# Kernel tuning notes

Hardware: AMD Instinct MI355X
Metric: run time of the kernel (lower is better)

Reference implementation:

```python
import jax, jax.numpy as jnp
import numpy as np

TOP_K = 2
NOISE_STDDEV = 1.0


def setup_inputs() -> dict:
    key = jax.random.key(0)
    k1, k2, k3, k4 = jax.random.split(key, 4)
    N, D, E = 16384, 2048, 64
    x = jax.random.normal(k1, (N, D), dtype=jnp.float32)
    W_gate = jax.random.normal(k2, (E, D), dtype=jnp.float32) * (1.0 / np.sqrt(D))
    W_noise = jax.random.normal(k3, (E, D), dtype=jnp.float32) * (1.0 / np.sqrt(D))
    noise = jax.random.normal(k4, (N, E), dtype=jnp.float32)
    return {"x": x, "W_gate": W_gate, "W_noise": W_noise, "noise": noise}


def reference(x, W_gate, W_noise, noise):
    # clean gating logits: [N, E]
    clean_logits = jnp.einsum("nd,ed->ne", x, W_gate)
    # noise scale via softplus of second projection (training mode)
    noise_scale = jax.nn.softplus(jnp.einsum("nd,ed->ne", x, W_noise))
    noisy_logits = clean_logits + noise_scale * noise * NOISE_STDDEV
    # top-k selection then softmax over the k selected logits
    top_k_logits, top_k_indices = jax.lax.top_k(noisy_logits, TOP_K)
    combined_weights = jax.nn.softmax(top_k_logits, axis=-1)
    return (combined_weights, top_k_indices, clean_logits)
```

## Files before the change

### kernel.cpp

```cpp
#include <hip/hip_runtime.h>
#include <math.h>


constexpr int NROWS = 16384;
constexpr int DDIM  = 2048;
constexpr int EDIM  = 64;
constexpr int BM    = 64;
constexpr int NKS   = 64;
constexpr int LSTR  = 132;
constexpr int IDX_OFF   = NROWS * 2;
constexpr int CLEAN_OFF = NROWS * 4;
constexpr size_t WPACK = 262144;
constexpr int BUFSZ = 24576;
constexpr int NBUF  = 4;

typedef _Float16 f16x8 __attribute__((ext_vector_type(8)));
typedef float    f32x4 __attribute__((ext_vector_type(4)));

__device__ __forceinline__ float softplus_f(float z) {
    return fmaxf(z, 0.0f) + log1pf(expf(-fabsf(z)));
}

__device__ __forceinline__ void gload16(const void* g, void* l) {
    __builtin_amdgcn_global_load_lds(
        (const __attribute__((address_space(1))) unsigned int*)g,
        (__attribute__((address_space(3))) unsigned int*)l, 16, 0, 0);
}

__global__ __launch_bounds__(256) void split_w_kernel(
    const float* __restrict__ Wg, const float* __restrict__ Wn,
    _Float16* __restrict__ wh, _Float16* __restrict__ wl)
{
    const int t    = blockIdx.x * 256 + threadIdx.x;
    const int grp  = t >> 6;
    const int lane = t & 63;
    const int kc   = grp >> 3;
    const int cg   = (grp >> 1) & 3;
    const int cf   = grp & 1;
    const int col  = cg * 32 + cf * 16 + (lane & 15);
    const int k0   = kc * 32 + (lane >> 4) * 8;
    const float* src = (col < 64) ? &Wg[(size_t)col * DDIM + k0]
                                  : &Wn[(size_t)(col - 64) * DDIM + k0];
    const float4 v0 = *reinterpret_cast<const float4*>(src);
    const float4 v1 = *reinterpret_cast<const float4*>(src + 4);
    float vv[8] = {v0.x, v0.y, v0.z, v0.w, v1.x, v1.y, v1.z, v1.w};
    union { _Float16 h[8]; uint4 u; } hh, ll;
    #pragma unroll
    for (int j = 0; j < 8; ++j) {
        hh.h[j] = (_Float16)vv[j];
        ll.h[j] = (_Float16)((vv[j] - (float)hh.h[j]) * 2048.0f);
    }
    const size_t off = (size_t)grp * 512 + lane * 8;
    *reinterpret_cast<uint4*>(&wh[off]) = hh.u;
    *reinterpret_cast<uint4*>(&wl[off]) = ll.u;
}

__device__ __forceinline__ void split8(const float4 a, const float4 b, f16x8& h, f16x8& l) {
    const float v[8] = {a.x, a.y, a.z, a.w, b.x, b.y, b.z, b.w};
    #pragma unroll
    for (int j = 0; j < 8; ++j) {
        const _Float16 hh = (_Float16)v[j];
        h[j] = hh;
        l[j] = (_Float16)((v[j] - (float)hh) * 2048.0f);
    }
}

__global__ __launch_bounds__(512, 1) void gating_mfma_kernel(
    const float* __restrict__ x,
    const float* __restrict__ noise,
    const _Float16* __restrict__ whp,
    const _Float16* __restrict__ wlp,
    float* __restrict__ out)
{
    extern __shared__ __align__(16) unsigned char smem[];

    const int tid = threadIdx.x;
    const int row_base = blockIdx.x * BM;
    const int lane = tid & 63;
    const int wid  = tid >> 6;
    const int g    = (lane >> 4) & 3;
    const int idx  = lane & 15;
    const int rg   = wid >> 2;
    const int cg   = wid & 3;

    const int sr  = tid >> 3;
    const int sq  = tid & 7;
    const int sq2 = sq ^ (sr & 7);
    const float* xsrc = x + (size_t)(row_base + sr) * DDIM + sq2 * 4;
    const char* bhsrc = (const char*)whp + tid * 16;
    const char* blsrc = (const char*)wlp + tid * 16;

    int aoff[2][2];
    #pragma unroll
    for (int rf = 0; rf < 2; ++rf) {
        const int row = rg * 32 + rf * 16 + idx;
        #pragma unroll
        for (int s = 0; s < 2; ++s)
            aoff[rf][s] = row * 128 + (((g * 2 + s) ^ (row & 7)) << 4);
    }
    int bhoff[2], bloff[2];
    #pragma unroll
    for (int cf = 0; cf < 2; ++cf) {
        bhoff[cf] = 8192  + (cg * 2 + cf) * 1024 + lane * 16;
        bloff[cf] = 16384 + (cg * 2 + cf) * 1024 + lane * 16;
    }

    f32x4 accm[2][2], accc[2][2];
    #pragma unroll
    for (int rf = 0; rf < 2; ++rf)
        #pragma unroll
        for (int cf = 0; cf < 2; ++cf) { accm[rf][cf] = (f32x4)0.0f; accc[rf][cf] = (f32x4)0.0f; }

    auto stage = [&](int u) {
        const int b = (u & (NBUF - 1)) * BUFSZ;
        gload16(xsrc + u * 32,                 smem + b + tid * 16);
        gload16(bhsrc + (size_t)u * 8192,      smem + b + 8192 + tid * 16);
        gload16(blsrc + (size_t)u * 8192,      smem + b + 16384 + tid * 16);
    };

    auto computeStep = [&](int b) {
        const float4 a00 = *reinterpret_cast<const float4*>(&smem[b + aoff[0][0]]);
        const float4 a01 = *reinterpret_cast<const float4*>(&smem[b + aoff[0][1]]);
        const float4 a10 = *reinterpret_cast<const float4*>(&smem[b + aoff[1][0]]);
        const float4 a11 = *reinterpret_cast<const float4*>(&smem[b + aoff[1][1]]);
        const f16x8 Bh0 = *reinterpret_cast<const f16x8*>(&smem[b + bhoff[0]]);
        const f16x8 Bh1 = *reinterpret_cast<const f16x8*>(&smem[b + bhoff[1]]);
        const f16x8 Bl0 = *reinterpret_cast<const f16x8*>(&smem[b + bloff[0]]);
        const f16x8 Bl1 = *reinterpret_cast<const f16x8*>(&smem[b + bloff[1]]);

        f16x8 Ah0, Al0, Ah1, Al1;
        split8(a00, a01, Ah0, Al0);
        split8(a10, a11, Ah1, Al1);

        accm[0][0] = __builtin_amdgcn_mfma_f32_16x16x32_f16(Ah0, Bh0, accm[0][0], 0, 0, 0);
        accm[0][1] = __builtin_amdgcn_mfma_f32_16x16x32_f16(Ah0, Bh1, accm[0][1], 0, 0, 0);
        accm[1][0] = __builtin_amdgcn_mfma_f32_16x16x32_f16(Ah1, Bh0, accm[1][0], 0, 0, 0);
        accm[1][1] = __builtin_amdgcn_mfma_f32_16x16x32_f16(Ah1, Bh1, accm[1][1], 0, 0, 0);
        accc[0][0] = __builtin_amdgcn_mfma_f32_16x16x32_f16(Al0, Bh0, accc[0][0], 0, 0, 0);
        accc[0][1] = __builtin_amdgcn_mfma_f32_16x16x32_f16(Al0, Bh1, accc[0][1], 0, 0, 0);
        accc[1][0] = __builtin_amdgcn_mfma_f32_16x16x32_f16(Al1, Bh0, accc[1][0], 0, 0, 0);
        accc[1][1] = __builtin_amdgcn_mfma_f32_16x16x32_f16(Al1, Bh1, accc[1][1], 0, 0, 0);
        accc[0][0] = __builtin_amdgcn_mfma_f32_16x16x32_f16(Ah0, Bl0, accc[0][0], 0, 0, 0);
        accc[0][1] = __builtin_amdgcn_mfma_f32_16x16x32_f16(Ah0, Bl1, accc[0][1], 0, 0, 0);
        accc[1][0] = __builtin_amdgcn_mfma_f32_16x16x32_f16(Ah1, Bl0, accc[1][0], 0, 0, 0);
        accc[1][1] = __builtin_amdgcn_mfma_f32_16x16x32_f16(Ah1, Bl1, accc[1][1], 0, 0, 0);
    };

    stage(0);
    stage(1);

    for (int t = 0; t < NKS - 2; ++t) {
        stage(t + 2);
        asm volatile("s_waitcnt vmcnt(6)" ::: "memory");
        __builtin_amdgcn_s_barrier();
        __builtin_amdgcn_sched_barrier(0);
        computeStep((t & (NBUF - 1)) * BUFSZ);
    }
    asm volatile("s_waitcnt vmcnt(3)" ::: "memory");
    __builtin_amdgcn_s_barrier();
    __builtin_amdgcn_sched_barrier(0);
    computeStep(((NKS - 2) & (NBUF - 1)) * BUFSZ);
    asm volatile("s_waitcnt vmcnt(0)" ::: "memory");
    __builtin_amdgcn_s_barrier();
    __builtin_amdgcn_sched_barrier(0);
    computeStep(((NKS - 1) & (NBUF - 1)) * BUFSZ);

    __builtin_amdgcn_s_barrier();

    float* L = reinterpret_cast<float*>(smem);
    #pragma unroll
    for (int rf = 0; rf < 2; ++rf)
        #pragma unroll
        for (int cf = 0; cf < 2; ++cf) {
            const int col = cg * 32 + cf * 16 + idx;
            #pragma unroll
            for (int q = 0; q < 4; ++q) {
                const int lrow = rg * 32 + rf * 16 + g * 4 + q;
                L[lrow * LSTR + col] = accm[rf][cf][q] + accc[rf][cf][q] * 4.8828125e-4f;
            }
        }
    __syncthreads();

    {
        const int row = tid >> 3;
        const int j   = tid & 7;
        const int e0  = j * 8;
        const int grow = row_base + row;

        const float4 c0 = *reinterpret_cast<const float4*>(&L[row * LSTR + e0]);
        const float4 c1 = *reinterpret_cast<const float4*>(&L[row * LSTR + e0 + 4]);
        const float4 s0 = *reinterpret_cast<const float4*>(&L[row * LSTR + 64 + e0]);
        const float4 s1 = *reinterpret_cast<const float4*>(&L[row * LSTR + 64 + e0 + 4]);
        *reinterpret_cast<float4*>(&out[CLEAN_OFF + (size_t)grow * EDIM + e0])     = c0;
        *reinterpret_cast<float4*>(&out[CLEAN_OFF + (size_t)grow * EDIM + e0 + 4]) = c1;

        const float4 z0 = *reinterpret_cast<const float4*>(&noise[(size_t)grow * EDIM + e0]);
        const float4 z1 = *reinterpret_cast<const float4*>(&noise[(size_t)grow * EDIM + e0 + 4]);

        float nv[8];
        nv[0] = fmaf(softplus_f(s0.x), z0.x, c0.x);
        nv[1] = fmaf(softplus_f(s0.y), z0.y, c0.y);
        nv[2] = fmaf(softplus_f(s0.z), z0.z, c0.z);
        nv[3] = fmaf(softplus_f(s0.w), z0.w, c0.w);
        nv[4] = fmaf(softplus_f(s1.x), z1.x, c1.x);
        nv[5] = fmaf(softplus_f(s1.y), z1.y, c1.y);
        nv[6] = fmaf(softplus_f(s1.z), z1.z, c1.z);
        nv[7] = fmaf(softplus_f(s1.w), z1.w, c1.w);

        float v0 = nv[0], v1 = -INFINITY;
        int   i0 = e0,    i1 = -1;
        #pragma unroll
        for (int m = 1; m < 8; ++m) {
            const float v = nv[m]; const int e = e0 + m;
            if (v > v0)      { v1 = v0; i1 = i0; v0 = v; i0 = e; }
            else if (v > v1) { v1 = v;  i1 = e; }
        }
        #pragma unroll
        for (int d = 1; d < 8; d <<= 1) {
            const float ov0 = __shfl_xor(v0, d); const int oi0 = __shfl_xor(i0, d);
            const float ov1 = __shfl_xor(v1, d); const int oi1 = __shfl_xor(i1, d);
            const bool aFirst = (v0 > ov0) || (v0 == ov0 && i0 < oi0);
            float n0, n1; int ni0, ni1;
            if (aFirst) {
                n0 = v0; ni0 = i0;
                const bool s = (v1 > ov0) || (v1 == ov0 && i1 < oi0);
                n1 = s ? v1 : ov0; ni1 = s ? i1 : oi0;
            } else {
                n0 = ov0; ni0 = oi0;
                const bool s = (ov1 > v0) || (ov1 == v0 && oi1 < i0);
                n1 = s ? ov1 : v0; ni1 = s ? oi1 : i0;
            }
            v0 = n0; i0 = ni0; v1 = n1; i1 = ni1;
        }
        if (j == 0) {
            const float ex = expf(v1 - v0);
            const float w0 = 1.0f / (1.0f + ex);
            const float w1 = 1.0f - w0;
            out[(size_t)grow * 2 + 0] = w0;
            out[(size_t)grow * 2 + 1] = w1;
            out[IDX_OFF + (size_t)grow * 2 + 0] = (float)i0;
            out[IDX_OFF + (size_t)grow * 2 + 1] = (float)i1;
        }
    }
}

extern "C" void kernel_launch(void* const* d_in, const int* in_sizes, int n_in,
                              void* d_out, int out_size, void* d_ws, size_t ws_size,
                              hipStream_t stream) {
    const float* x     = (const float*)d_in[0];
    const float* Wg    = (const float*)d_in[1];
    const float* Wn    = (const float*)d_in[2];
    const float* noise = (const float*)d_in[3];
    float* out = (float*)d_out;

    _Float16* wh = (_Float16*)d_ws;
    _Float16* wl = wh + WPACK;

    split_w_kernel<<<dim3(128), dim3(256), 0, stream>>>(Wg, Wn, wh, wl);
    gating_mfma_kernel<<<dim3(NROWS / BM), dim3(512), NBUF * BUFSZ, stream>>>(x, noise, wh, wl, out);
}
```

Measured before the change: 53.92 us.

## Software-pipeline LDS fragment reads with MFMA compute using five-buffer ring

Each LDS fragment read for step t+1 is now issued before the MFMA compute of step t, using two register fragment sets that alternate, so LDS latency overlaps with matrix work. To keep buffers safe with the deeper read-ahead, the ring grows from four to five stages with explicit rotating offsets, and the loop is unrolled by two. This costs more registers and more LDS (120KB), which could affect scheduling, but occupancy is already one block per CU.

Measured after the change: 54.57 us. No clear change (+1.2%).

```diff
diff --git a/kernel.cpp b/kernel.cpp
--- a/kernel.cpp
+++ b/kernel.cpp
@@ -12,7 +12,8 @@
 constexpr int CLEAN_OFF = NROWS * 4;
 constexpr size_t WPACK = 262144;
 constexpr int BUFSZ = 24576;
-constexpr int NBUF  = 4;
+constexpr int NBUF  = 5;
+constexpr int LDSSZ = NBUF * BUFSZ;
 
 typedef _Float16 f16x8 __attribute__((ext_vector_type(8)));
 typedef float    f32x4 __attribute__((ext_vector_type(4)));
@@ -65,6 +66,11 @@
     }
 }
 
+struct Frags {
+    float4 a00, a01, a10, a11;
+    f16x8  bh0, bh1, bl0, bl1;
+};
+
 __global__ __launch_bounds__(512, 1) void gating_mfma_kernel(
     const float* __restrict__ x,
     const float* __restrict__ noise,
@@ -95,8 +101,8 @@
     for (int rf = 0; rf < 2; ++rf) {
         const int row = rg * 32 + rf * 16 + idx;
         #pragma unroll
-        for (int s = 0; s < 2; ++s)
-            aoff[rf][s] = row * 128 + (((g * 2 + s) ^ (row & 7)) << 4);
+        for (int j = 0; j < 2; ++j)
+            aoff[rf][j] = row * 128 + (((g * 2 + j) ^ (row & 7)) << 4);
     }
     int bhoff[2], bloff[2];
     #pragma unroll
@@ -111,59 +117,90 @@
         #pragma unroll
         for (int cf = 0; cf < 2; ++cf) { accm[rf][cf] = (f32x4)0.0f; accc[rf][cf] = (f32x4)0.0f; }
 
-    auto stage = [&](int u) {
-        const int b = (u & (NBUF - 1)) * BUFSZ;
-        gload16(xsrc + u * 32,                 smem + b + tid * 16);
-        gload16(bhsrc + (size_t)u * 8192,      smem + b + 8192 + tid * 16);
-        gload16(blsrc + (size_t)u * 8192,      smem + b + 16384 + tid * 16);
+    auto stage = [&](int u, int b) {
+        gload16(xsrc + u * 32,                smem + b + tid * 16);
+        gload16(bhsrc + (size_t)u * 8192,     smem + b + 8192  + tid * 16);
+        gload16(blsrc + (size_t)u * 8192,     smem + b + 16384 + tid * 16);
     };
 
-    auto computeStep = [&](int b) {
-        const float4 a00 = *reinterpret_cast<const float4*>(&smem[b + aoff[0][0]]);
-        const float4 a01 = *reinterpret_cast<const float4*>(&smem[b + aoff[0][1]]);
-        const float4 a10 = *reinterpret_cast<const float4*>(&smem[b + aoff[1][0]]);
-        const float4 a11 = *reinterpret_cast<const float4*>(&smem[b + aoff[1][1]]);
-        const f16x8 Bh0 = *reinterpret_cast<const f16x8*>(&smem[b + bhoff[0]]);
-        const f16x8 Bh1 = *reinterpret_cast<const f16x8*>(&smem[b + bhoff[1]]);
-        const f16x8 Bl0 = *reinterpret_cast<const f16x8*>(&smem[b + bloff[0]]);
-        const f16x8 Bl1 = *reinterpret_cast<const f16x8*>(&smem[b + bloff[1]]);
-
+    auto readFrags = [&](int b, Frags& f) {
+        f.a00 = *reinterpret_cast<const float4*>(&smem[b + aoff[0][0]]);
+        f.a01 = *reinterpret_cast<const float4*>(&smem[b + aoff[0][1]]);
+        f.a10 = *reinterpret_cast<const float4*>(&smem[b + aoff[1][0]]);
+        f.a11 = *reinterpret_cast<const float4*>(&smem[b + aoff[1][1]]);
+        f.bh0 = *reinterpret_cast<const f16x8*>(&smem[b + bhoff[0]]);
+        f.bh1 = *reinterpret_cast<const f16x8*>(&smem[b + bhoff[1]]);
+        f.bl0 = *reinterpret_cast<const f16x8*>(&smem[b + bloff[0]]);
+        f.bl1 = *reinterpret_cast<const f16x8*>(&smem[b + bloff[1]]);
+    };
+
+    auto computeF = [&](const Frags& f) {
         f16x8 Ah0, Al0, Ah1, Al1;
-        split8(a00, a01, Ah0, Al0);
-        split8(a10, a11, Ah1, Al1);
-
-        accm[0][0] = __builtin_amdgcn_mfma_f32_16x16x32_f16(Ah0, Bh0, accm[0][0], 0, 0, 0);
-        accm[0][1] = __builtin_amdgcn_mfma_f32_16x16x32_f16(Ah0, Bh1, accm[0][1], 0, 0, 0);
-        accm[1][0] = __builtin_amdgcn_mfma_f32_16x16x32_f16(Ah1, Bh0, accm[1][0], 0, 0, 0);
-        accm[1][1] = __builtin_amdgcn_mfma_f32_16x16x32_f16(Ah1, Bh1, accm[1][1], 0, 0, 0);
-        accc[0][0] = __builtin_amdgcn_mfma_f32_16x16x32_f16(Al0, Bh0, accc[0][0], 0, 0, 0);
-        accc[0][1] = __builtin_amdgcn_mfma_f32_16x16x32_f16(Al0, Bh1, accc[0][1], 0, 0, 0);
-        accc[1][0] = __builtin_amdgcn_mfma_f32_16x16x32_f16(Al1, Bh0, accc[1][0], 0, 0, 0);
-        accc[1][1] = __builtin_amdgcn_mfma_f32_16x16x32_f16(Al1, Bh1, accc[1][1], 0, 0, 0);
-        accc[0][0] = __builtin_amdgcn_mfma_f32_16x16x32_f16(Ah0, Bl0, accc[0][0], 0, 0, 0);
-        accc[0][1] = __builtin_amdgcn_mfma_f32_16x16x32_f16(Ah0, Bl1, accc[0][1], 0, 0, 0);
-        accc[1][0] = __builtin_amdgcn_mfma_f32_16x16x32_f16(Ah1, Bl0, accc[1][0], 0, 0, 0);
-        accc[1][1] = __builtin_amdgcn_mfma_f32_16x16x32_f16(Ah1, Bl1, accc[1][1], 0, 0, 0);
+        split8(f.a00, f.a01, Ah0, Al0);
+        split8(f.a10, f.a11, Ah1, Al1);
+        accm[0][0] = __builtin_amdgcn_mfma_f32_16x16x32_f16(Ah0, f.bh0, accm[0][0], 0, 0, 0);
+        accm[0][1] = __builtin_amdgcn_mfma_f32_16x16x32_f16(Ah0, f.bh1, accm[0][1], 0, 0, 0);
+        accm[1][0] = __builtin_amdgcn_mfma_f32_16x16x32_f16(Ah1, f.bh0, accm[1][0], 0, 0, 0);
+        accm[1][1] = __builtin_amdgcn_mfma_f32_16x16x32_f16(Ah1, f.bh1, accm[1][1], 0, 0, 0);
+        accc[0][0] = __builtin_amdgcn_mfma_f32_16x16x32_f16(Al0, f.bh0, accc[0][0], 0, 0, 0);
+        accc[0][1] = __builtin_amdgcn_mfma_f32_16x16x32_f16(Al0, f.bh1, accc[0][1], 0, 0, 0);
+        accc[1][0] = __builtin_amdgcn_mfma_f32_16x16x32_f16(Al1, f.bh0, accc[1][0], 0, 0, 0);
+        accc[1][1] = __builtin_amdgcn_mfma_f32_16x16x32_f16(Al1, f.bh1, accc[1][1], 0, 0, 0);
+        accc[0][0] = __builtin_amdgcn_mfma_f32_16x16x32_f16(Ah0, f.bl0, accc[0][0], 0, 0, 0);
+        accc[0][1] = __builtin_amdgcn_mfma_f32_16x16x32_f16(Ah0, f.bl1, accc[0][1], 0, 0, 0);
+        accc[1][0] = __builtin_amdgcn_mfma_f32_16x16x32_f16(Ah1, f.bl0, accc[1][0], 0, 0, 0);
+        accc[1][1] = __builtin_amdgcn_mfma_f32_16x16x32_f16(Ah1, f.bl1, accc[1][1], 0, 0, 0);
     };
 
-    stage(0);
-    stage(1);
-
-    for (int t = 0; t < NKS - 2; ++t) {
-        stage(t + 2);
+    Frags f0, f1;
+
+    stage(0, 0);
+    stage(1, BUFSZ);
+    stage(2, 2 * BUFSZ);
+    asm volatile("s_waitcnt vmcnt(6)" ::: "memory");
+    __builtin_amdgcn_s_barrier();
+    __builtin_amdgcn_sched_barrier(0);
+    readFrags(0, f0);
+
+    int wb = 3 * BUFSZ;
+    int rb = 1 * BUFSZ;
+    for (int tt = 0; tt < 30; ++tt) {
+        stage(2 * tt + 3, wb);
+        wb += BUFSZ; if (wb == LDSSZ) wb = 0;
         asm volatile("s_waitcnt vmcnt(6)" ::: "memory");
         __builtin_amdgcn_s_barrier();
         __builtin_amdgcn_sched_barrier(0);
-        computeStep((t & (NBUF - 1)) * BUFSZ);
-    }
+        readFrags(rb, f1);
+        rb += BUFSZ; if (rb == LDSSZ) rb = 0;
+        computeF(f0);
+        stage(2 * tt + 4, wb);
+        wb += BUFSZ; if (wb == LDSSZ) wb = 0;
+        asm volatile("s_waitcnt vmcnt(6)" ::: "memory");
+        __builtin_amdgcn_s_barrier();
+        __builtin_amdgcn_sched_barrier(0);
+        readFrags(rb, f0);
+        rb += BUFSZ; if (rb == LDSSZ) rb = 0;
+        computeF(f1);
+    }
+    stage(63, wb);
+    asm volatile("s_waitcnt vmcnt(6)" ::: "memory");
+    __builtin_amdgcn_s_barrier();
+    __builtin_amdgcn_sched_barrier(0);
+    readFrags(rb, f1);
+    rb += BUFSZ; if (rb == LDSSZ) rb = 0;
+    computeF(f0);
     asm volatile("s_waitcnt vmcnt(3)" ::: "memory");
     __builtin_amdgcn_s_barrier();
     __builtin_amdgcn_sched_barrier(0);
-    computeStep(((NKS - 2) & (NBUF - 1)) * BUFSZ);
+    readFrags(rb, f0);
+    rb += BUFSZ; if (rb == LDSSZ) rb = 0;
+    computeF(f1);
     asm volatile("s_waitcnt vmcnt(0)" ::: "memory");
     __builtin_amdgcn_s_barrier();
     __builtin_amdgcn_sched_barrier(0);
-    computeStep(((NKS - 1) & (NBUF - 1)) * BUFSZ);
+    readFrags(rb, f1);
+    computeF(f0);
+    computeF(f1);
 
     __builtin_amdgcn_s_barrier();
 
@@ -257,5 +294,5 @@
     _Float16* wl = wh + WPACK;
 
     split_w_kernel<<<dim3(128), dim3(256), 0, stream>>>(Wg, Wn, wh, wl);
-    gating_mfma_kernel<<<dim3(NROWS / BM), dim3(512), NBUF * BUFSZ, stream>>>(x, noise, wh, wl, out);
-}
+    gating_mfma_kernel<<<dim3(NROWS / BM), dim3(512), LDSSZ, stream>>>(x, noise, wh, wl, out);
+}
```

## Convert x tiles to split fp16 once in LDS, pipelined one step ahead

Applied to the files above, without the earlier changes.

Each 64x32 x tile is now staged as fp32 into a double buffer, and every thread converts its own 4 floats into hi/lo fp16 pieces. These are written to a separate swizzled fp16 buffer one k-step before the MFMA step that consumes them. This removes the duplicated split work, since 4 column-group waves each split the same A fragment, and it shrinks the A LDS reads to f16x8. The cost is an extra LDS write and read round trip per step, more LDS use, and a restructured waitcnt/barrier schedule in which conversion and compute share a single barrier.

Measured after the change: 70.04 us. 29.9% more time.

```diff
diff --git a/kernel.cpp b/kernel.cpp
--- a/kernel.cpp
+++ b/kernel.cpp
@@ -11,8 +11,13 @@
 constexpr int IDX_OFF   = NROWS * 2;
 constexpr int CLEAN_OFF = NROWS * 4;
 constexpr size_t WPACK = 262144;
-constexpr int BUFSZ = 24576;
-constexpr int NBUF  = 4;
+constexpr int XS    = 8192;
+constexpr int XSBASE = 0;
+constexpr int XF    = 8192;
+constexpr int XFBASE = 16384;
+constexpr int WBUF  = 16384;
+constexpr int WBASE = 32768;
+constexpr int LDSSZ = 98304;
 
 typedef _Float16 f16x8 __attribute__((ext_vector_type(8)));
 typedef float    f32x4 __attribute__((ext_vector_type(4)));
@@ -55,16 +60,6 @@
     *reinterpret_cast<uint4*>(&wl[off]) = ll.u;
 }
 
-__device__ __forceinline__ void split8(const float4 a, const float4 b, f16x8& h, f16x8& l) {
-    const float v[8] = {a.x, a.y, a.z, a.w, b.x, b.y, b.z, b.w};
-    #pragma unroll
-    for (int j = 0; j < 8; ++j) {
-        const _Float16 hh = (_Float16)v[j];
-        h[j] = hh;
-        l[j] = (_Float16)((v[j] - (float)hh) * 2048.0f);
-    }
-}
-
 __global__ __launch_bounds__(512, 1) void gating_mfma_kernel(
     const float* __restrict__ x,
     const float* __restrict__ noise,
@@ -83,26 +78,29 @@
     const int rg   = wid >> 2;
     const int cg   = wid & 3;
 
-    const int sr  = tid >> 3;
-    const int sq  = tid & 7;
-    const int sq2 = sq ^ (sr & 7);
-    const float* xsrc = x + (size_t)(row_base + sr) * DDIM + sq2 * 4;
+    const float* xsrc = x + (size_t)(row_base + (tid >> 3)) * DDIM + (tid & 7) * 4;
     const char* bhsrc = (const char*)whp + tid * 16;
     const char* blsrc = (const char*)wlp + tid * 16;
 
-    int aoff[2][2];
+    const int sr = tid >> 3;
+    const int kq = tid & 7;
+    const int ks = kq >> 1;
+    const int hf = (kq & 1) * 8;
+    const int woff_h = sr * 128 + ((ks ^ (sr & 7)) << 4) + hf;
+    const int woff_l = sr * 128 + (((4 + ks) ^ (sr & 7)) << 4) + hf;
+
+    int aoff_h[2], aoff_l[2];
     #pragma unroll
     for (int rf = 0; rf < 2; ++rf) {
         const int row = rg * 32 + rf * 16 + idx;
-        #pragma unroll
-        for (int s = 0; s < 2; ++s)
-            aoff[rf][s] = row * 128 + (((g * 2 + s) ^ (row & 7)) << 4);
+        aoff_h[rf] = row * 128 + (((g) ^ (row & 7)) << 4);
+        aoff_l[rf] = row * 128 + (((4 + g) ^ (row & 7)) << 4);
     }
     int bhoff[2], bloff[2];
     #pragma unroll
     for (int cf = 0; cf < 2; ++cf) {
-        bhoff[cf] = 8192  + (cg * 2 + cf) * 1024 + lane * 16;
-        bloff[cf] = 16384 + (cg * 2 + cf) * 1024 + lane * 16;
+        bhoff[cf] = (cg * 2 + cf) * 1024 + lane * 16;
+        bloff[cf] = 8192 + (cg * 2 + cf) * 1024 + lane * 16;
     }
 
     f32x4 accm[2][2], accc[2][2];
@@ -112,25 +110,38 @@
         for (int cf = 0; cf < 2; ++cf) { accm[rf][cf] = (f32x4)0.0f; accc[rf][cf] = (f32x4)0.0f; }
 
     auto stage = [&](int u) {
-        const int b = (u & (NBUF - 1)) * BUFSZ;
-        gload16(xsrc + u * 32,                 smem + b + tid * 16);
-        gload16(bhsrc + (size_t)u * 8192,      smem + b + 8192 + tid * 16);
-        gload16(blsrc + (size_t)u * 8192,      smem + b + 16384 + tid * 16);
+        gload16(xsrc + u * 32, smem + XSBASE + (u & 1) * XS + tid * 16);
+        const int wb = WBASE + (u & 3) * WBUF;
+        gload16(bhsrc + (size_t)u * 8192, smem + wb + tid * 16);
+        gload16(blsrc + (size_t)u * 8192, smem + wb + 8192 + tid * 16);
     };
 
-    auto computeStep = [&](int b) {
-        const float4 a00 = *reinterpret_cast<const float4*>(&smem[b + aoff[0][0]]);
-        const float4 a01 = *reinterpret_cast<const float4*>(&smem[b + aoff[0][1]]);
-        const float4 a10 = *reinterpret_cast<const float4*>(&smem[b + aoff[1][0]]);
-        const float4 a11 = *reinterpret_cast<const float4*>(&smem[b + aoff[1][1]]);
-        const f16x8 Bh0 = *reinterpret_cast<const f16x8*>(&smem[b + bhoff[0]]);
-        const f16x8 Bh1 = *reinterpret_cast<const f16x8*>(&smem[b + bhoff[1]]);
-        const f16x8 Bl0 = *reinterpret_cast<const f16x8*>(&smem[b + bloff[0]]);
-        const f16x8 Bl1 = *reinterpret_cast<const f16x8*>(&smem[b + bloff[1]]);
-
-        f16x8 Ah0, Al0, Ah1, Al1;
-        split8(a00, a01, Ah0, Al0);
-        split8(a10, a11, Ah1, Al1);
+    auto convert = [&](int u) {
+        const float4 v = *reinterpret_cast<const float4*>(
+            &smem[XSBASE + (u & 1) * XS + tid * 16]);
+        const int bf = XFBASE + (u & 1) * XF;
+        union { _Float16 h[4]; uint2 q; } hh, ll;
+        const float vv[4] = {v.x, v.y, v.z, v.w};
+        #pragma unroll
+        for (int j = 0; j < 4; ++j) {
+            hh.h[j] = (_Float16)vv[j];
+            ll.h[j] = (_Float16)((vv[j] - (float)hh.h[j]) * 2048.0f);
+        }
+        *reinterpret_cast<uint2*>(&smem[bf + woff_h]) = hh.q;
+        *reinterpret_cast<uint2*>(&smem[bf + woff_l]) = ll.q;
+    };
+
+    auto compute = [&](int t) {
+        const int bf = XFBASE + (t & 1) * XF;
+        const int wb = WBASE + (t & 3) * WBUF;
+        const f16x8 Ah0 = *reinterpret_cast<const f16x8*>(&smem[bf + aoff_h[0]]);
+        const f16x8 Al0 = *reinterpret_cast<const f16x8*>(&smem[bf + aoff_l[0]]);
+        const f16x8 Ah1 = *reinterpret_cast<const f16x8*>(&smem[bf + aoff_h[1]]);
+        const f16x8 Al1 = *reinterpret_cast<const f16x8*>(&smem[bf + aoff_l[1]]);
+        const f16x8 Bh0 = *reinterpret_cast<const f16x8*>(&smem[wb + bhoff[0]]);
+        const f16x8 Bh1 = *reinterpret_cast<const f16x8*>(&smem[wb + bhoff[1]]);
+        const f16x8 Bl0 = *reinterpret_cast<const f16x8*>(&smem[wb + bloff[0]]);
+        const f16x8 Bl1 = *reinterpret_cast<const f16x8*>(&smem[wb + bloff[1]]);
 
         accm[0][0] = __builtin_amdgcn_mfma_f32_16x16x32_f16(Ah0, Bh0, accm[0][0], 0, 0, 0);
         accm[0][1] = __builtin_amdgcn_mfma_f32_16x16x32_f16(Ah0, Bh1, accm[0][1], 0, 0, 0);
@@ -148,24 +159,23 @@
 
     stage(0);
     stage(1);
-
-    for (int t = 0; t < NKS - 2; ++t) {
-        stage(t + 2);
-        asm volatile("s_waitcnt vmcnt(6)" ::: "memory");
+    asm volatile("s_waitcnt vmcnt(5)" ::: "memory");
+    convert(0);
+
+    for (int t = 0; t < NKS; ++t) {
+        if (t < NKS - 1) {
+            asm volatile("s_waitcnt vmcnt(2) lgkmcnt(0)" ::: "memory");
+        } else {
+            asm volatile("s_waitcnt vmcnt(0) lgkmcnt(0)" ::: "memory");
+        }
         __builtin_amdgcn_s_barrier();
         __builtin_amdgcn_sched_barrier(0);
-        computeStep((t & (NBUF - 1)) * BUFSZ);
-    }
-    asm volatile("s_waitcnt vmcnt(3)" ::: "memory");
-    __builtin_amdgcn_s_barrier();
-    __builtin_amdgcn_sched_barrier(0);
-    computeStep(((NKS - 2) & (NBUF - 1)) * BUFSZ);
-    asm volatile("s_waitcnt vmcnt(0)" ::: "memory");
-    __builtin_amdgcn_s_barrier();
-    __builtin_amdgcn_sched_barrier(0);
-    computeStep(((NKS - 1) & (NBUF - 1)) * BUFSZ);
-
-    __builtin_amdgcn_s_barrier();
+        if (t < NKS - 2) stage(t + 2);
+        if (t < NKS - 1) convert(t + 1);
+        compute(t);
+    }
+
+    __syncthreads();
 
     float* L = reinterpret_cast<float*>(smem);
     #pragma unroll
@@ -257,5 +267,5 @@
     _Float16* wl = wh + WPACK;
 
     split_w_kernel<<<dim3(128), dim3(256), 0, stream>>>(Wg, Wn, wh, wl);
-    gating_mfma_kernel<<<dim3(NROWS / BM), dim3(512), NBUF * BUFSZ, stream>>>(x, noise, wh, wl, out);
-}
+    gating_mfma_kernel<<<dim3(NROWS / BM), dim3(512), LDSSZ, stream>>>(x, noise, wh, wl, out);
+}
```
